# Optimization experiments

Measured on AMD Instinct MI355X. Metric: run time of the kernel, lower is better.

Reference implementation:

```python
import jax, jax.numpy as jnp
import numpy as np

TEMPERATURE = 0.1
EPS = 1e-08
NEG_INF = -9e15


def setup_inputs() -> dict:
    key = jax.random.key(0)
    k1, k2 = jax.random.split(key)
    B, D = 4096, 256
    z_i = jax.random.normal(k1, (B, D), dtype=jnp.float32)
    z_j = jax.random.normal(k2, (B, D), dtype=jnp.float32)
    mask_positive = jnp.ones((B,), dtype=bool)
    return {"z_i": z_i, "z_j": z_j, "mask_positive": mask_positive}


def reference(z_i, z_j, mask_positive):
    B = z_i.shape[0]
    N = 2 * B
    z = jnp.concatenate([z_i, z_j], axis=0)  # [N, D]
    # cosine similarity: normalize (norms clamped to eps) then GEMM
    norms = jnp.maximum(jnp.linalg.norm(z, axis=1, keepdims=True), EPS)
    zn = z / norms
    sim = jnp.matmul(zn, zn.T) / TEMPERATURE  # [N, N]
    # mask self-similarity on diagonal
    rows = jnp.arange(N)
    sim = sim.at[rows, rows].set(NEG_INF)
    logprob = jax.nn.log_softmax(sim, axis=1)
    # positive of row k is row (k+B) mod N
    positives = jnp.concatenate([jnp.arange(B, N), jnp.arange(0, B)])
    loss_vec = -logprob[rows, positives]  # [N]
    mp = jnp.concatenate([mask_positive, mask_positive])  # [N] bool
    cnt = jnp.sum(mp.astype(jnp.float32))
    total = jnp.sum(jnp.where(mp, loss_vec, 0.0))
    loss = jnp.where(cnt > 0, total / jnp.maximum(cnt, 1.0), 0.0)
    return loss
```

## Files before the change

### kernel.cpp

```cpp
#include <hip/hip_runtime.h>
#include <hip/hip_bf16.h>

#define NTOT   8192
#define BHALF  4096
#define DDIM   256
#define SMOD   32
#define NPART  4
#define MAXSLOT 5
#define EXPSCALE 14.4269504088896341f

typedef __attribute__((ext_vector_type(8))) short bf16x8_t;
typedef __attribute__((ext_vector_type(4))) float f32x4_t;

__device__ inline unsigned short f2bf(float x) {
    __hip_bfloat16 h = __float2bfloat16(x);
    return __builtin_bit_cast(unsigned short, h);
}

__global__ void norm_pair_kernel(const float* __restrict__ zi,
                                 const float* __restrict__ zj,
                                 unsigned short* __restrict__ zn,
                                 float* __restrict__ posdot,
                                 float* __restrict__ s_part) {
    int gtid = blockIdx.x * 256 + threadIdx.x;
    if (gtid < NTOT * NPART) s_part[gtid] = 0.0f;
    int k    = gtid >> 6;
    int lane = gtid & 63;
    float4 vi = reinterpret_cast<const float4*>(zi + (size_t)k * DDIM)[lane];
    float4 vj = reinterpret_cast<const float4*>(zj + (size_t)k * DDIM)[lane];
    float ssi = vi.x*vi.x + vi.y*vi.y + vi.z*vi.z + vi.w*vi.w;
    float ssj = vj.x*vj.x + vj.y*vj.y + vj.z*vj.z + vj.w*vj.w;
    float dot = vi.x*vj.x + vi.y*vj.y + vi.z*vj.z + vi.w*vj.w;
    #pragma unroll
    for (int off = 32; off >= 1; off >>= 1) {
        ssi += __shfl_xor(ssi, off);
        ssj += __shfl_xor(ssj, off);
        dot += __shfl_xor(dot, off);
    }
    float ri = 1.0f / fmaxf(sqrtf(ssi), 1e-8f);
    float rj = 1.0f / fmaxf(sqrtf(ssj), 1e-8f);
    ushort4 oi, oj;
    oi.x = f2bf(vi.x * ri); oi.y = f2bf(vi.y * ri);
    oi.z = f2bf(vi.z * ri); oi.w = f2bf(vi.w * ri);
    oj.x = f2bf(vj.x * rj); oj.y = f2bf(vj.y * rj);
    oj.z = f2bf(vj.z * rj); oj.w = f2bf(vj.w * rj);
    reinterpret_cast<ushort4*>(zn + (size_t)k * DDIM)[lane] = oi;
    reinterpret_cast<ushort4*>(zn + (size_t)(k + BHALF) * DDIM)[lane] = oj;
    if (lane == 0) posdot[k] = dot * ri * rj * 10.0f;
}

__global__ void __launch_bounds__(256)
gemm_sym_kernel(const unsigned short* __restrict__ zn,
                float* __restrict__ s_part) {
    __shared__ unsigned short ldsB[64 * 256];
    __shared__ float colLDS[MAXSLOT][4][64];

    const int tid  = threadIdx.x;
    const int lane = tid & 63;
    const int wv   = tid >> 6;
    const int m    = lane & 15;
    const int quad = lane >> 4;
    const int biA  = blockIdx.x;
    const int s    = blockIdx.y;

    float* rowPart = s_part + (size_t)(s   & (NPART - 1)) * NTOT;
    float* colPart = s_part + (size_t)(biA & (NPART - 1)) * NTOT;

    int slot = 0;
    #pragma unroll
    for (int p = 0; p < 2; ++p) {
        const int bi = p ? (63 - biA) : biA;
        const int R0 = bi << 7;
        const int cs0 = 2 * bi + ((s - 2 * bi) & (SMOD - 1));
        if (cs0 >= 128) continue;

        bf16x8_t afrag[2][8];
        #pragma unroll
        for (int rf = 0; rf < 2; ++rf) {
            const unsigned short* arow = zn + (size_t)(R0 + wv*32 + rf*16 + m) * DDIM;
            #pragma unroll
            for (int kk = 0; kk < 8; ++kk)
                afrag[rf][kk] = *reinterpret_cast<const bf16x8_t*>(arow + kk*32 + quad*8);
        }

        float rowacc[2][4] = {{0.f,0.f,0.f,0.f},{0.f,0.f,0.f,0.f}};

        for (int cs = cs0; cs < 128; cs += SMOD) {
            const int C0 = cs << 6;
            const bool isDiag = ((cs >> 1) == bi);

            __syncthreads();
            #pragma unroll
            for (int t = 0; t < 8; ++t) {
                int ci = t * 256 + tid;
                int r = ci >> 5, c = ci & 31;
                bf16x8_t v = *reinterpret_cast<const bf16x8_t*>(
                                 zn + (size_t)(C0 + r) * DDIM + c * 8);
                *reinterpret_cast<bf16x8_t*>(&ldsB[r * 256 + ((c ^ (r & 7)) << 3)]) = v;
            }
            __syncthreads();

            #pragma unroll
            for (int cf = 0; cf < 4; ++cf) {
                f32x4_t c0 = (f32x4_t){0.f,0.f,0.f,0.f};
                f32x4_t c1 = (f32x4_t){0.f,0.f,0.f,0.f};
                #pragma unroll
                for (int kk = 0; kk < 8; ++kk) {
                    bf16x8_t b = *reinterpret_cast<const bf16x8_t*>(
                        &ldsB[(cf*16 + m) * 256 + (((kk*4 + quad) ^ (m & 7)) << 3)]);
                    c0 = __builtin_amdgcn_mfma_f32_16x16x32_bf16(afrag[0][kk], b, c0, 0, 0, 0);
                    c1 = __builtin_amdgcn_mfma_f32_16x16x32_bf16(afrag[1][kk], b, c1, 0, 0, 0);
                }
                const int gc = C0 + cf*16 + m;
                float colsum = 0.f;
                #pragma unroll
                for (int r = 0; r < 4; ++r) {
                    int gr0 = R0 + wv*32 + quad*4 + r;
                    float e0 = exp2f(c0[r] * EXPSCALE);
                    float e1 = exp2f(c1[r] * EXPSCALE);
                    if (isDiag && gr0 == gc)        e0 = 0.f;
                    if (isDiag && (gr0 + 16) == gc) e1 = 0.f;
                    rowacc[0][r] += e0;
                    rowacc[1][r] += e1;
                    colsum += e0 + e1;
                }
                if (!isDiag) {
                    colsum += __shfl_xor(colsum, 16);
                    colsum += __shfl_xor(colsum, 32);
                    if (quad == 0) colLDS[slot][wv][cf*16 + m] = colsum;
                }
            }
            ++slot;
        }

        #pragma unroll
        for (int rf = 0; rf < 2; ++rf)
            #pragma unroll
            for (int r = 0; r < 4; ++r) {
                float v = rowacc[rf][r];
                v += __shfl_xor(v, 1);
                v += __shfl_xor(v, 2);
                v += __shfl_xor(v, 4);
                v += __shfl_xor(v, 8);
                if (m == 0)
                    atomicAdd(&rowPart[R0 + wv*32 + rf*16 + quad*4 + r], v);
            }
    }

    __syncthreads();

    if (tid < 64) {
        int slot2 = 0;
        #pragma unroll
        for (int p = 0; p < 2; ++p) {
            const int bi = p ? (63 - biA) : biA;
            const int cs0 = 2 * bi + ((s - 2 * bi) & (SMOD - 1));
            if (cs0 >= 128) continue;
            for (int cs = cs0; cs < 128; cs += SMOD) {
                if ((cs >> 1) != bi) {
                    float v = colLDS[slot2][0][tid] + colLDS[slot2][1][tid]
                            + colLDS[slot2][2][tid] + colLDS[slot2][3][tid];
                    atomicAdd(&colPart[(cs << 6) + tid], v);
                }
                ++slot2;
            }
        }
    }
}

__global__ void finalize_kernel(const float* __restrict__ s_part,
                                const float* __restrict__ posdot,
                                const unsigned char* __restrict__ mask,
                                float* __restrict__ out) {
    int tid = threadIdx.x, lane = tid & 63, wv = tid >> 6;
    float tot = 0.f, cnt = 0.f;
    #pragma unroll
    for (int si = 0; si < NTOT / 1024; ++si) {
        int k = si * 1024 + tid;
        int kb = k & (BHALF - 1);
        if (mask[kb] != 0) {
            float sk = s_part[k] + s_part[NTOT + k]
                     + s_part[2*NTOT + k] + s_part[3*NTOT + k];
            tot += __logf(sk) - posdot[kb];
            cnt += 1.f;
        }
    }
    #pragma unroll
    for (int off = 32; off >= 1; off >>= 1) {
        tot += __shfl_xor(tot, off);
        cnt += __shfl_xor(cnt, off);
    }
    __shared__ float st[16], sc[16];
    if (lane == 0) { st[wv] = tot; sc[wv] = cnt; }
    __syncthreads();
    if (tid == 0) {
        float T = 0.f, C = 0.f;
        #pragma unroll
        for (int i = 0; i < 16; ++i) { T += st[i]; C += sc[i]; }
        out[0] = (C > 0.f) ? (T / fmaxf(C, 1.f)) : 0.f;
    }
}

extern "C" void kernel_launch(void* const* d_in, const int* in_sizes, int n_in,
                              void* d_out, int out_size, void* d_ws, size_t ws_size,
                              hipStream_t stream) {
    const float* zi = (const float*)d_in[0];
    const float* zj = (const float*)d_in[1];
    const unsigned char* mask = (const unsigned char*)d_in[2];
    float* out = (float*)d_out;

    unsigned short* zn = (unsigned short*)d_ws;
    float* s_part = (float*)((char*)d_ws + (size_t)NTOT * DDIM * 2);
    float* posdot = s_part + NPART * NTOT;

    norm_pair_kernel<<<dim3(1024), dim3(256), 0, stream>>>(zi, zj, zn, posdot, s_part);
    gemm_sym_kernel<<<dim3(32, SMOD), dim3(256), 0, stream>>>(zn, s_part);
    finalize_kernel<<<dim3(1), dim3(1024), 0, stream>>>(s_part, posdot, mask, out);
}
```

Before: 122.6 us.

## Replace symmetric GEMM with full GEMM and register-prefetched B tiles

Drops the symmetric upper-triangle scheme, which computed each off-diagonal tile once and credited both row and column sums through atomics. Each block now computes a full 128x512 strip of the similarity matrix and accumulates row sums only. The next B tile is prefetched into registers while the current one is consumed, to overlap global loads with MFMA work. This roughly doubles the matrix-multiply and exp work but removes the column reduction, the colLDS staging and the uneven per-block workload.

```diff
diff --git a/kernel.cpp b/kernel.cpp
--- a/kernel.cpp
+++ b/kernel.cpp
@@ -4,9 +4,7 @@
 #define NTOT   8192
 #define BHALF  4096
 #define DDIM   256
-#define SMOD   32
 #define NPART  4
-#define MAXSLOT 5
 #define EXPSCALE 14.4269504088896341f
 
 typedef __attribute__((ext_vector_type(8))) short bf16x8_t;
@@ -50,122 +48,101 @@
 }
 
 __global__ void __launch_bounds__(256)
-gemm_sym_kernel(const unsigned short* __restrict__ zn,
-                float* __restrict__ s_part) {
+gemm_kernel(const unsigned short* __restrict__ zn,
+            float* __restrict__ s_part) {
     __shared__ unsigned short ldsB[64 * 256];
-    __shared__ float colLDS[MAXSLOT][4][64];
 
     const int tid  = threadIdx.x;
     const int lane = tid & 63;
     const int wv   = tid >> 6;
     const int m    = lane & 15;
     const int quad = lane >> 4;
-    const int biA  = blockIdx.x;
+    const int bi   = blockIdx.x;
     const int s    = blockIdx.y;
+    const int R0   = bi << 7;
+    const int CB   = s << 9;
 
-    float* rowPart = s_part + (size_t)(s   & (NPART - 1)) * NTOT;
-    float* colPart = s_part + (size_t)(biA & (NPART - 1)) * NTOT;
+    float* rowPart = s_part + (size_t)(s & (NPART - 1)) * NTOT;
 
-    int slot = 0;
+    bf16x8_t afrag[2][8];
     #pragma unroll
-    for (int p = 0; p < 2; ++p) {
-        const int bi = p ? (63 - biA) : biA;
-        const int R0 = bi << 7;
-        const int cs0 = 2 * bi + ((s - 2 * bi) & (SMOD - 1));
-        if (cs0 >= 128) continue;
+    for (int rf = 0; rf < 2; ++rf) {
+        const unsigned short* arow = zn + (size_t)(R0 + wv*32 + rf*16 + m) * DDIM;
+        #pragma unroll
+        for (int kk = 0; kk < 8; ++kk)
+            afrag[rf][kk] = *reinterpret_cast<const bf16x8_t*>(arow + kk*32 + quad*8);
+    }
 
-        bf16x8_t afrag[2][8];
+    bf16x8_t pf[8];
+    #pragma unroll
+    for (int t = 0; t < 8; ++t) {
+        int ci = t * 256 + tid;
+        int r = ci >> 5, c = ci & 31;
+        pf[t] = *reinterpret_cast<const bf16x8_t*>(zn + (size_t)(CB + r) * DDIM + c * 8);
+    }
+
+    float rowacc[2][4] = {{0.f,0.f,0.f,0.f},{0.f,0.f,0.f,0.f}};
+
+    for (int it = 0; it < 8; ++it) {
+        const int C0 = CB + it * 64;
+        const bool isDiag = ((C0 >> 7) == bi);
+
+        __syncthreads();
         #pragma unroll
-        for (int rf = 0; rf < 2; ++rf) {
-            const unsigned short* arow = zn + (size_t)(R0 + wv*32 + rf*16 + m) * DDIM;
-            #pragma unroll
-            for (int kk = 0; kk < 8; ++kk)
-                afrag[rf][kk] = *reinterpret_cast<const bf16x8_t*>(arow + kk*32 + quad*8);
+        for (int t = 0; t < 8; ++t) {
+            int ci = t * 256 + tid;
+            int r = ci >> 5, c = ci & 31;
+            *reinterpret_cast<bf16x8_t*>(&ldsB[r * 256 + ((c ^ (r & 7)) << 3)]) = pf[t];
         }
+        __syncthreads();
 
-        float rowacc[2][4] = {{0.f,0.f,0.f,0.f},{0.f,0.f,0.f,0.f}};
-
-        for (int cs = cs0; cs < 128; cs += SMOD) {
-            const int C0 = cs << 6;
-            const bool isDiag = ((cs >> 1) == bi);
-
-            __syncthreads();
+        if (it < 7) {
             #pragma unroll
             for (int t = 0; t < 8; ++t) {
                 int ci = t * 256 + tid;
                 int r = ci >> 5, c = ci & 31;
-                bf16x8_t v = *reinterpret_cast<const bf16x8_t*>(
-                                 zn + (size_t)(C0 + r) * DDIM + c * 8);
-                *reinterpret_cast<bf16x8_t*>(&ldsB[r * 256 + ((c ^ (r & 7)) << 3)]) = v;
+                pf[t] = *reinterpret_cast<const bf16x8_t*>(
+                            zn + (size_t)(C0 + 64 + r) * DDIM + c * 8);
             }
-            __syncthreads();
-
-            #pragma unroll
-            for (int cf = 0; cf < 4; ++cf) {
-                f32x4_t c0 = (f32x4_t){0.f,0.f,0.f,0.f};
-                f32x4_t c1 = (f32x4_t){0.f,0.f,0.f,0.f};
-                #pragma unroll
-                for (int kk = 0; kk < 8; ++kk) {
-                    bf16x8_t b = *reinterpret_cast<const bf16x8_t*>(
-                        &ldsB[(cf*16 + m) * 256 + (((kk*4 + quad) ^ (m & 7)) << 3)]);
-                    c0 = __builtin_amdgcn_mfma_f32_16x16x32_bf16(afrag[0][kk], b, c0, 0, 0, 0);
-                    c1 = __builtin_amdgcn_mfma_f32_16x16x32_bf16(afrag[1][kk], b, c1, 0, 0, 0);
-                }
-                const int gc = C0 + cf*16 + m;
-                float colsum = 0.f;
-                #pragma unroll
-                for (int r = 0; r < 4; ++r) {
-                    int gr0 = R0 + wv*32 + quad*4 + r;
-                    float e0 = exp2f(c0[r] * EXPSCALE);
-                    float e1 = exp2f(c1[r] * EXPSCALE);
-                    if (isDiag && gr0 == gc)        e0 = 0.f;
-                    if (isDiag && (gr0 + 16) == gc) e1 = 0.f;
-                    rowacc[0][r] += e0;
-                    rowacc[1][r] += e1;
-                    colsum += e0 + e1;
-                }
-                if (!isDiag) {
-                    colsum += __shfl_xor(colsum, 16);
-                    colsum += __shfl_xor(colsum, 32);
-                    if (quad == 0) colLDS[slot][wv][cf*16 + m] = colsum;
-                }
-            }
-            ++slot;
         }
 
         #pragma unroll
-        for (int rf = 0; rf < 2; ++rf)
+        for (int cf = 0; cf < 4; ++cf) {
+            f32x4_t c0 = (f32x4_t){0.f,0.f,0.f,0.f};
+            f32x4_t c1 = (f32x4_t){0.f,0.f,0.f,0.f};
+            #pragma unroll
+            for (int kk = 0; kk < 8; ++kk) {
+                bf16x8_t b = *reinterpret_cast<const bf16x8_t*>(
+                    &ldsB[(cf*16 + m) * 256 + (((kk*4 + quad) ^ (m & 7)) << 3)]);
+                c0 = __builtin_amdgcn_mfma_f32_16x16x32_bf16(afrag[0][kk], b, c0, 0, 0, 0);
+                c1 = __builtin_amdgcn_mfma_f32_16x16x32_bf16(afrag[1][kk], b, c1, 0, 0, 0);
+            }
+            const int gc = C0 + cf*16 + m;
             #pragma unroll
             for (int r = 0; r < 4; ++r) {
-                float v = rowacc[rf][r];
-                v += __shfl_xor(v, 1);
-                v += __shfl_xor(v, 2);
-                v += __shfl_xor(v, 4);
-                v += __shfl_xor(v, 8);
-                if (m == 0)
-                    atomicAdd(&rowPart[R0 + wv*32 + rf*16 + quad*4 + r], v);
-            }
-    }
-
-    __syncthreads();
-
-    if (tid < 64) {
-        int slot2 = 0;
-        #pragma unroll
-        for (int p = 0; p < 2; ++p) {
-            const int bi = p ? (63 - biA) : biA;
-            const int cs0 = 2 * bi + ((s - 2 * bi) & (SMOD - 1));
-            if (cs0 >= 128) continue;
-            for (int cs = cs0; cs < 128; cs += SMOD) {
-                if ((cs >> 1) != bi) {
-                    float v = colLDS[slot2][0][tid] + colLDS[slot2][1][tid]
-                            + colLDS[slot2][2][tid] + colLDS[slot2][3][tid];
-                    atomicAdd(&colPart[(cs << 6) + tid], v);
-                }
-                ++slot2;
+                int gr0 = R0 + wv*32 + quad*4 + r;
+                float e0 = exp2f(c0[r] * EXPSCALE);
+                float e1 = exp2f(c1[r] * EXPSCALE);
+                if (isDiag && gr0 == gc)        e0 = 0.f;
+                if (isDiag && (gr0 + 16) == gc) e1 = 0.f;
+                rowacc[0][r] += e0;
+                rowacc[1][r] += e1;
             }
         }
     }
+
+    #pragma unroll
+    for (int rf = 0; rf < 2; ++rf)
+        #pragma unroll
+        for (int r = 0; r < 4; ++r) {
+            float v = rowacc[rf][r];
+            v += __shfl_xor(v, 1);
+            v += __shfl_xor(v, 2);
+            v += __shfl_xor(v, 4);
+            v += __shfl_xor(v, 8);
+            if (m == 0)
+                atomicAdd(&rowPart[R0 + wv*32 + rf*16 + quad*4 + r], v);
+        }
 }
 
 __global__ void finalize_kernel(const float* __restrict__ s_part,
@@ -214,6 +191,6 @@
     float* posdot = s_part + NPART * NTOT;
 
     norm_pair_kernel<<<dim3(1024), dim3(256), 0, stream>>>(zi, zj, zn, posdot, s_part);
-    gemm_sym_kernel<<<dim3(32, SMOD), dim3(256), 0, stream>>>(zn, s_part);
+    gemm_kernel<<<dim3(64, 16), dim3(256), 0, stream>>>(zn, s_part);
     finalize_kernel<<<dim3(1), dim3(1024), 0, stream>>>(s_part, posdot, mask, out);
 }
```

Result: faster. 119.3 us (-2.7%).
